# Performance work log

Measured on AMD Instinct MI355X. Metric: run time of the kernel, lower is better.

The kernel has to match this reference:

```python
import jax, jax.numpy as jnp
import numpy as np

P = 1024          # number of projection angles
N = 64            # harmonic order -> 2N+1 = 129 basis functions
K = 7             # temporal basis order -> K+1 = 8 functions
NUM_INSTANCES = 8
L_OUT = 256       # native temporal-function length
M = 512           # g_t.shape[-2]
NB = 2 * N + 1


def _interp_linear(f, out_len):
    # torch F.interpolate(mode='linear', align_corners=False) on a 1D signal f: [L]
    L = f.shape[-1]
    x = (jnp.arange(out_len, dtype=f.dtype) + 0.5) * (L / out_len) - 0.5
    x = jnp.clip(x, 0.0, L - 1)
    x0 = jnp.floor(x).astype(jnp.int32)
    x1 = jnp.minimum(x0 + 1, L - 1)
    w = x - x0.astype(f.dtype)
    return f[x0] * (1.0 - w) + f[x1] * w


def setup_inputs() -> dict:
    key = jax.random.key(0)
    k1, k2, k3 = jax.random.split(key, 3)
    g_t = jax.random.normal(k1, (1, 1, M, 2 * P), dtype=jnp.float32)
    temporal_fcts = jax.random.normal(k2, (1, K + 1, L_OUT), dtype=jnp.float32)
    theta = jax.random.uniform(k3, (P,), dtype=jnp.float32) * jnp.pi
    return {"g_t": g_t, "temporal_fcts": temporal_fcts, "theta": theta}


def reference(g_t, temporal_fcts, theta):
    g_c = g_t.astype(jnp.complex64)                       # [1,1,M,2P]
    n_idx = jnp.arange(NB, dtype=jnp.float32) - N         # (n - N)
    # Theta_mtx[p,n] = exp(1j*(n-N)*theta[p]); symm uses (theta - pi)
    Theta = jnp.exp(1j * n_idx[None, :] * theta[:, None])             # [P, NB] complex64
    Theta_s = jnp.exp(1j * n_idx[None, :] * (theta[:, None] - jnp.pi))  # [P, NB]
    # psi_mtx[k,p]: interpolate each temporal function from L_OUT -> P samples
    psi = jax.vmap(lambda f: _interp_linear(f, P))(temporal_fcts[0])  # [K+1, P] real
    psi_c = psi.astype(jnp.complex64)
    # L1[p, n*(K+1)+k] = Theta[p,n] * psi[k,p]  (top block); symm block below
    top = (Theta[:, :, None] * psi_c.T[:, None, :]).reshape(P, NB * (K + 1))
    bot = (Theta_s[:, :, None] * psi_c.T[:, None, :]).reshape(P, NB * (K + 1))
    L1 = jnp.concatenate([top, bot], axis=0)              # [2P, NB*(K+1)]
    eta = jnp.linalg.pinv(L1) @ jnp.swapaxes(g_c, 2, 3)   # [1,1,NB*(K+1),M]
    g_est = L1 @ eta                                      # [1,1,2P,M]
    # b[m,n,p] = sum_k eta[0,0,n*(K+1)+k,m] * psi[k,p]
    eta_r = eta[0, 0].reshape(NB, K + 1, M)
    b = jnp.einsum('nkm,kp->mnp', eta_r, psi_c)           # [M, NB, P]
    # f_pol_est_s[m,p,i] = sum_n b[m,n, i*P//I] * Theta[p,n]
    sel = (jnp.arange(NUM_INSTANCES) * P) // NUM_INSTANCES
    f_pol_est_s = jnp.einsum('mni,pn->mpi', b[:, :, sel], Theta)  # [M, P, I]
    psi_mtx = psi_c[None]                                  # [1, K+1, P]
    return eta, L1, jnp.swapaxes(g_est, 2, 3), b, f_pol_est_s, psi_mtx
```

## Files before the change

kernel.cpp:

```cpp
#include <hip/hip_runtime.h>

#define NQ 1032
#define NE 520
#define NO 512

#define C_ETA 0
#define C_L1  1056768
#define C_G   5283840
#define C_B   7380992
#define C_F   142647296
#define C_PSI 151035904
#define C_TOTAL 151052288

#define R_ETA 0
#define R_L1  528384
#define R_G   2641920
#define R_B   3690496
#define R_F   71323648
#define R_PSI 75517952

#define SL_PSI32 0
#define SL_THC32 9216
#define SL_THS32 142336
#define SL_BSEL  275456
#define SL_TOTALF 1332224

#define SB_PSI64 0
#define SB_THC64 69632
#define SB_THS64 1130496
#define SB_CT    2191360
#define SB_A0    2262016
#define SB_B0    6592512
#define SB_B1    10856448
#define SB_INVD  15054848
#define SB_LT    15059008
#define SB_RZ    19851328
#define SB_TOTAL 24643648

__device__ inline void tri_it(int e, int& i, int& t){
  i = 0; int base = 0;
  while (base + i + 1 <= e){ base += i + 1; ++i; }
  t = e - base;
}

__global__ __launch_bounds__(256) void k_prep(const float* tf, const float* theta,
    float* psi32, double* psi64, double* thc64, double* ths64,
    float* thc32, float* ths32, float* o_psi, int cpx){
  int idx = blockIdx.x*256 + threadIdx.x;
  if (idx < 8192){
    int k = idx >> 10, p = idx & 1023;
    double x = 0.25*(double)p - 0.375;
    x = fmin(fmax(x, 0.0), 255.0);
    int x0 = (int)x;
    int x1 = min(x0+1, 255);
    double w = x - (double)x0;
    double v = (double)tf[k*256+x0]*(1.0-w) + (double)tf[k*256+x1]*w;
    psi64[k*1024+p] = v;
    float vf = (float)v;
    psi32[k*1024+p] = vf;
    if (cpx){ o_psi[idx*2+0] = vf; o_psi[idx*2+1] = 0.f; }
    else    { o_psi[idx] = vf; }
  } else {
    int j = idx - 8192;
    if (j < 129*1024){
      int n = j >> 10, p = j & 1023;
      double a = (double)(n-64)*(double)theta[p];
      double c = cos(a), s = sin(a);
      thc64[j] = c; ths64[j] = s;
      thc32[j] = (float)c; ths32[j] = (float)s;
    }
  }
}

__global__ __launch_bounds__(256) void k_l1out(const float* tf, const float* theta,
    float* out_l1, int cpx){
  int row = blockIdx.x; int p = row & 1023; int bot = row >> 10;
  __shared__ float cc[129], ss[129], pp[8];
  int tid = threadIdx.x;
  float th = theta[p];
  if (tid < 129){
    float a = (float)(tid - 64) * th;
    cc[tid] = cosf(a); ss[tid] = sinf(a);
  }
  if (tid >= 192 && tid < 200){
    int k = tid - 192;
    float x = 0.25f*(float)p - 0.375f;
    x = fminf(fmaxf(x, 0.f), 255.f);
    int x0 = (int)x;
    int x1 = min(x0+1, 255);
    float w = x - (float)x0;
    pp[k] = tf[k*256+x0]*(1.f-w) + tf[k*256+x1]*w;
  }
  __syncthreads();
  for (int q = tid; q < NQ; q += 256){
    int n = q >> 3, k = q & 7;
    float sg = (bot && (n & 1)) ? -1.f : 1.f;
    float w = pp[k]*sg;
    if (cpx) ((float2*)out_l1)[(size_t)row*NQ + q] = make_float2(cc[n]*w, ss[n]*w);
    else     out_l1[(size_t)row*NQ + q] = cc[n]*w;
  }
}

__global__ __launch_bounds__(256) void k_ctab(const float* theta, const double* psi64, double2* C){
  int t = blockIdx.x; double dd = 2.0*(double)t;
  __shared__ double cs[1024], sn[1024];
  __shared__ double red[4][2];
  int tid = threadIdx.x;
  for (int p = tid; p < 1024; p += 256){ double a = dd*(double)theta[p]; cs[p] = cos(a); sn[p] = sin(a); }
  __syncthreads();
  int lane = tid & 63, wid = tid >> 6;
  for (int k = 0; k < 8; ++k) for (int k2 = k; k2 < 8; ++k2){
    double sr = 0, si = 0;
    for (int p = tid; p < 1024; p += 256){
      double w = psi64[k*1024+p]*psi64[k2*1024+p];
      sr += cs[p]*w; si += sn[p]*w;
    }
    for (int o = 32; o > 0; o >>= 1){ sr += __shfl_down(sr, o, 64); si += __shfl_down(si, o, 64); }
    if (lane == 0){ red[wid][0] = sr; red[wid][1] = si; }
    __syncthreads();
    if (tid == 0){
      double R = red[0][0]+red[1][0]+red[2][0]+red[3][0];
      double I = red[0][1]+red[1][1]+red[2][1]+red[3][1];
      C[t*64 + k*8 + k2] = make_double2(R, I);
      C[t*64 + k2*8 + k] = make_double2(R, I);
    }
    __syncthreads();
  }
}

__global__ __launch_bounds__(256) void k_afill(const double2* C, double2* A){
  int idx = blockIdx.x*256 + threadIdx.x;
  if (idx >= NE*NE) return;
  int r = idx / NE, cix = idx - r*NE;
  int k = r & 7, i = r >> 3, j = cix >> 3, k2 = cix & 7;
  int dt = j - i;
  double2 v;
  if (dt >= 0){ v = C[dt*64 + k*8 + k2]; v.x *= 2.0; v.y *= 2.0; }
  else { v = C[(-dt)*64 + k*8 + k2]; v.x *= 2.0; v.y *= -2.0; }
  A[idx] = v;
}

__global__ __launch_bounds__(256) void k_bgemm(const float* g, const double* thc64, const double* ths64,
    const double* psi64, double2* B0, double2* B1){
  int n = blockIdx.x; int m0 = blockIdx.y * 128;
  int par = n & 1;
  __shared__ float u[64][129];
  __shared__ double cs[64], sn[64], ps[8][64];
  int tid = threadIdx.x;
  int k = tid >> 5, mg = tid & 31;
  double ar[4] = {0,0,0,0}, ai[4] = {0,0,0,0};
  for (int p0 = 0; p0 < 1024; p0 += 64){
    __syncthreads();
    if (tid < 64){ cs[tid] = thc64[n*1024 + p0 + tid]; sn[tid] = ths64[n*1024 + p0 + tid]; }
    for (int e = tid; e < 512; e += 256){ int kk = e >> 6, pp = e & 63; ps[kk][pp] = psi64[kk*1024 + p0 + pp]; }
    for (int e = tid; e < 2048; e += 256){
      int m = e >> 4, p4 = (e & 15) * 4;
      const float4 a = *(const float4*)(g + (size_t)(m0+m)*2048 + p0 + p4);
      const float4 b = *(const float4*)(g + (size_t)(m0+m)*2048 + 1024 + p0 + p4);
      float4 uu;
      if (par){ uu.x = a.x-b.x; uu.y = a.y-b.y; uu.z = a.z-b.z; uu.w = a.w-b.w; }
      else    { uu.x = a.x+b.x; uu.y = a.y+b.y; uu.z = a.z+b.z; uu.w = a.w+b.w; }
      u[p4+0][m] = uu.x; u[p4+1][m] = uu.y; u[p4+2][m] = uu.z; u[p4+3][m] = uu.w;
    }
    __syncthreads();
    for (int p = 0; p < 64; ++p){
      double w = ps[k][p];
      double wr = cs[p]*w, wi = sn[p]*w;
      #pragma unroll
      for (int j = 0; j < 4; ++j){
        double uu = (double)u[p][mg + 32*j];
        ar[j] += wr*uu; ai[j] -= wi*uu;
      }
    }
  }
  int hr = (n >> 1)*8 + k;
  double2* B = par ? B1 : B0;
  #pragma unroll
  for (int j = 0; j < 4; ++j) B[(size_t)hr*512 + m0 + mg + 32*j] = make_double2(ar[j], ai[j]);
}

__global__ __launch_bounds__(256) void k_potrf(double2* A, double* invd, int j0){
  __shared__ double2 T[2145];
  int tid = threadIdx.x;
  for (int e = tid; e < 2145; e += 256){
    int i, t; tri_it(e, i, t);
    T[e] = A[(size_t)(j0+i)*NE + j0 + t];
  }
  __syncthreads();
  for (int j = 0; j < 65; ++j){
    double inv = 1.0 / T[(j*(j+1))/2 + j].x;
    int i = j + 1 + (tid & 63);
    if (i < 65){
      double2 lij = T[(i*(i+1))/2 + j];
      for (int t = j+1+(tid>>6); t <= i; t += 4){
        double2 ltj = T[(t*(t+1))/2 + j];
        double2 a = T[(i*(i+1))/2 + t];
        a.x -= (lij.x*ltj.x + lij.y*ltj.y)*inv;
        a.y -= (lij.y*ltj.x - lij.x*ltj.y)*inv;
        T[(i*(i+1))/2 + t] = a;
      }
    }
    __syncthreads();
  }
  for (int e = tid; e < 2145; e += 256){
    int i, t; tri_it(e, i, t);
    double dinv = 1.0 / sqrt(T[(t*(t+1))/2 + t].x);
    double2 v = T[e]; v.x *= dinv; v.y *= dinv;
    A[(size_t)(j0+i)*NE + j0 + t] = v;
    if (i == t) invd[j0+i] = dinv;
  }
}

__global__ __launch_bounds__(256) void k_trsm(double2* A, const double* invd, int j0){
  int lane = threadIdx.x & 63, wid = threadIdx.x >> 6;
  int rg = j0 + 65 + blockIdx.x*4 + wid;
  if (rg >= NE) return;
  double2 a0 = A[(size_t)rg*NE + j0 + lane];
  double2 a64 = (lane == 0) ? A[(size_t)rg*NE + j0 + 64] : make_double2(0,0);
  for (int c = 0; c < 65; ++c){
    double xr, xi;
    if (c < 64){ xr = __shfl(a0.x, c, 64); xi = __shfl(a0.y, c, 64); }
    else { xr = __shfl(a64.x, 0, 64); xi = __shfl(a64.y, 0, 64); }
    double iv = invd[j0 + c];
    xr *= iv; xi *= iv;
    if (c < 64){ if (lane == c){ a0.x = xr; a0.y = xi; } }
    else if (lane == 0){ a64.x = xr; a64.y = xi; }
    if (lane > c){
      double2 l = A[(size_t)(j0+lane)*NE + j0 + c];
      a0.x -= xr*l.x + xi*l.y; a0.y -= xi*l.x - xr*l.y;
    }
    if (lane == 0 && c < 64){
      double2 l = A[(size_t)(j0+64)*NE + j0 + c];
      a64.x -= xr*l.x + xi*l.y; a64.y -= xi*l.x - xr*l.y;
    }
  }
  A[(size_t)rg*NE + j0 + lane] = a0;
  if (lane == 0) A[(size_t)rg*NE + j0 + 64] = a64;
}

__global__ __launch_bounds__(256) void k_syrk(double2* A, int j0){
  if (blockIdx.y > blockIdx.x) return;
  int j1 = j0 + 65;
  int i0 = j1 + blockIdx.x*32, t0 = j1 + blockIdx.y*32;
  __shared__ double2 Li[32][17];
  __shared__ double2 Lt[32][17];
  int tid = threadIdx.x;
  int oi = tid >> 3, tj = (tid & 7)*4;
  double2 acc[4] = {make_double2(0,0),make_double2(0,0),make_double2(0,0),make_double2(0,0)};
  for (int c0 = 0; c0 < 65; c0 += 16){
    int cw = min(16, 65 - c0);
    __syncthreads();
    for (int e = tid; e < 512; e += 256){
      int r = e >> 4, c = e & 15;
      double2 zi = make_double2(0,0), zt = zi;
      if (c < cw){
        if (i0 + r < NE) zi = A[(size_t)(i0+r)*NE + j0 + c0 + c];
        if (t0 + r < NE) zt = A[(size_t)(t0+r)*NE + j0 + c0 + c];
      }
      Li[r][c] = zi; Lt[r][c] = zt;
    }
    __syncthreads();
    for (int c = 0; c < cw; ++c){
      double2 li = Li[oi][c];
      #pragma unroll
      for (int j = 0; j < 4; ++j){
        double2 lt = Lt[tj+j][c];
        acc[j].x += li.x*lt.x + li.y*lt.y;
        acc[j].y += li.y*lt.x - li.x*lt.y;
      }
    }
  }
  int gi = i0 + oi;
  if (gi < NE){
    #pragma unroll
    for (int j = 0; j < 4; ++j){
      int gt = t0 + tj + j;
      if (gt < NE && gt <= gi){
        double2 v = A[(size_t)gi*NE + gt];
        v.x -= acc[j].x; v.y -= acc[j].y;
        A[(size_t)gi*NE + gt] = v;
      }
    }
  }
}

__global__ __launch_bounds__(256) void k_tr(const double2* A, double2* LT){
  __shared__ double2 tl[32][33];
  int bc = blockIdx.x*32;
  int bt = blockIdx.y*32;
  int lx = threadIdx.x & 31, ly = threadIdx.x >> 5;
  #pragma unroll
  for (int rr = 0; rr < 32; rr += 8){
    int t = bt + ly + rr, c = bc + lx;
    double2 v = make_double2(0,0);
    if (t < NE && c < NE && t > c) v = A[(size_t)t*NE + c];
    tl[ly+rr][lx] = v;
  }
  __syncthreads();
  #pragma unroll
  for (int rr = 0; rr < 32; rr += 8){
    int c = bc + ly + rr, t = bt + lx;
    if (c < NE) LT[(size_t)c*576 + t] = tl[lx][ly+rr];
  }
}

__global__ __launch_bounds__(256) void k_rz(const double2* A, double2* RZ){
  int idx = blockIdx.x*256 + threadIdx.x;
  if (idx >= NE*576) return;
  int c = idx / 576, t = idx - c*576;
  double2 v = (t < c) ? A[(size_t)c*NE + t] : make_double2(0,0);
  RZ[idx] = v;
}

__global__ __launch_bounds__(256) void k_solve(const double2* LT, const double2* RZ,
                                               const double* invd,
                                               double2* B0, double2* B1){
  int tid = threadIdx.x; int lane = tid & 63; int wid = tid >> 6;
  int w = blockIdx.x*4 + wid;
  int sys = (w >= 256) ? 1 : 0;
  int c0 = (sys ? (w - 256) : w) * 2;
  int n = sys ? NO : NE;
  double2* B = sys ? B1 : B0;
  double2 y[9][2];
  #pragma unroll
  for (int r = 0; r < 9; ++r){
    int t = r*64 + lane;
    #pragma unroll
    for (int j = 0; j < 2; ++j)
      y[r][j] = (t < n) ? B[(size_t)t*512 + c0 + j] : make_double2(0,0);
  }

  double2 Lc[9], Ln[9];

  #pragma unroll
  for (int r = 0; r < 9; ++r) Lc[r] = LT[(size_t)0*576 + r*64 + lane];
  #pragma unroll
  for (int rr = 0; rr < 9; ++rr){
    if (rr*64 < n){
      int cend = min(n, rr*64 + 64);
      for (int c = rr*64; c < cend; ++c){
        if (c + 1 < n){
          #pragma unroll
          for (int r = 0; r < 9; ++r) Ln[r] = LT[(size_t)(c+1)*576 + r*64 + lane];
        }
        int la = c & 63;
        double iv = invd[c];
        double xr[2], xi[2];
        #pragma unroll
        for (int j = 0; j < 2; ++j){
          xr[j] = __shfl(y[rr][j].x, la, 64)*iv;
          xi[j] = __shfl(y[rr][j].y, la, 64)*iv;
        }
        if (lane == la){
          #pragma unroll
          for (int j = 0; j < 2; ++j){ y[rr][j].x = xr[j]; y[rr][j].y = xi[j]; }
        }
        #pragma unroll
        for (int r = 0; r < 9; ++r){
          if (r >= rr){
            double2 l = Lc[r];
            #pragma unroll
            for (int j = 0; j < 2; ++j){
              y[r][j].x -= l.x*xr[j] - l.y*xi[j];
              y[r][j].y -= l.x*xi[j] + l.y*xr[j];
            }
          }
        }
        #pragma unroll
        for (int r = 0; r < 9; ++r) Lc[r] = Ln[r];
      }
    }
  }

  #pragma unroll
  for (int r = 0; r < 9; ++r) Lc[r] = RZ[(size_t)(n-1)*576 + r*64 + lane];
  #pragma unroll
  for (int rr = 8; rr >= 0; --rr){
    if (rr*64 < n){
      int cstart = min(n, rr*64 + 64) - 1;
      for (int c = cstart; c >= rr*64; --c){
        if (c > 0){
          #pragma unroll
          for (int r = 0; r < 9; ++r) Ln[r] = RZ[(size_t)(c-1)*576 + r*64 + lane];
        }
        int la = c & 63;
        double iv = invd[c];
        double xr[2], xi[2];
        #pragma unroll
        for (int j = 0; j < 2; ++j){
          xr[j] = __shfl(y[rr][j].x, la, 64)*iv;
          xi[j] = __shfl(y[rr][j].y, la, 64)*iv;
        }
        if (lane == la){
          #pragma unroll
          for (int j = 0; j < 2; ++j){ y[rr][j].x = xr[j]; y[rr][j].y = xi[j]; }
        }
        #pragma unroll
        for (int r = 0; r < 9; ++r){
          if (r <= rr){
            double2 l = Lc[r];
            #pragma unroll
            for (int j = 0; j < 2; ++j){
              y[r][j].x -= l.x*xr[j] + l.y*xi[j];
              y[r][j].y -= l.x*xi[j] - l.y*xr[j];
            }
          }
        }
        #pragma unroll
        for (int r = 0; r < 9; ++r) Lc[r] = Ln[r];
      }
    }
  }

  #pragma unroll
  for (int r = 0; r < 9; ++r){
    int t = r*64 + lane;
    if (t < n){
      #pragma unroll
      for (int j = 0; j < 2; ++j) B[(size_t)t*512 + c0 + j] = y[r][j];
    }
  }
}

__global__ __launch_bounds__(256) void k_eta(const double2* B0, const double2* B1,
                                             float* out_eta, int cpx){
  int idx = blockIdx.x*256 + threadIdx.x;
  if (idx >= NQ*512) return;
  int q = idx >> 9;
  int m = idx & 511;
  int n = q >> 3, k = q & 7;
  const double2* B = (n & 1) ? B1 : B0;
  int hr = (n >> 1)*8 + k;
  double2 v = B[(size_t)hr*512 + m];
  if (cpx) ((float2*)out_eta)[idx] = make_float2((float)v.x, (float)v.y);
  else     out_eta[idx] = (float)v.x;
}

__global__ __launch_bounds__(256) void k_gestb(const double2* B0, const double2* B1,
    const float* psi32, const float* thc32, const float* ths32,
    float* out_b, float* out_g, float2* BSEL, int cpx){
  int m = blockIdx.x; int p = blockIdx.y*256 + threadIdx.x;
  __shared__ float4 eL4[516];
  float2* eL2 = (float2*)eL4;
  for (int e = threadIdx.x; e < NQ; e += 256){
    int n = e >> 3, k = e & 7;
    const double2* B = (n & 1) ? B1 : B0;
    double2 v = B[(size_t)((n >> 1)*8 + k)*512 + m];
    eL2[e] = make_float2((float)v.x, (float)v.y);
  }
  __syncthreads();
  float pr[8];
  #pragma unroll
  for (int k = 0; k < 8; ++k) pr[k] = psi32[k*1024+p];
  float aEx=0, aEy=0, aOx=0, aOy=0;
  size_t bbase = (size_t)m*129*1024 + p;
  for (int n = 0; n < 129; ++n){
    float c = thc32[n*1024+p], s = ths32[n*1024+p];
    float4 e0 = eL4[n*4+0], e1 = eL4[n*4+1], e2 = eL4[n*4+2], e3 = eL4[n*4+3];
    float br = e0.x*pr[0] + e0.z*pr[1] + e1.x*pr[2] + e1.z*pr[3]
             + e2.x*pr[4] + e2.z*pr[5] + e3.x*pr[6] + e3.z*pr[7];
    float bi = e0.y*pr[0] + e0.w*pr[1] + e1.y*pr[2] + e1.w*pr[3]
             + e2.y*pr[4] + e2.w*pr[5] + e3.y*pr[6] + e3.w*pr[7];
    if (cpx) ((float2*)out_b)[bbase + (size_t)n*1024] = make_float2(br, bi);
    else     out_b[bbase + (size_t)n*1024] = br;
    if ((p & 127) == 0) BSEL[(size_t)m*NQ + n*8 + (p >> 7)] = make_float2(br, bi);
    float tr = c*br - s*bi, ti = c*bi + s*br;
    if (n & 1){ aOx += tr; aOy += ti; } else { aEx += tr; aEy += ti; }
  }
  if (cpx){
    ((float2*)out_g)[(size_t)m*2048 + p]        = make_float2(aEx+aOx, aEy+aOy);
    ((float2*)out_g)[(size_t)m*2048 + p + 1024] = make_float2(aEx-aOx, aEy-aOy);
  } else {
    out_g[(size_t)m*2048 + p]        = aEx+aOx;
    out_g[(size_t)m*2048 + p + 1024] = aEx-aOx;
  }
}

__global__ __launch_bounds__(256) void k_fpol(const float2* BSEL, const float* thc32,
    const float* ths32, float* out_f, int cpx){
  int m = blockIdx.x; int p = blockIdx.y*256 + threadIdx.x;
  __shared__ float4 bs4[516];
  float2* bs2 = (float2*)bs4;
  for (int e = threadIdx.x; e < NQ; e += 256) bs2[e] = BSEL[(size_t)m*NQ + e];
  __syncthreads();
  float ar[8] = {0,0,0,0,0,0,0,0}, ai[8] = {0,0,0,0,0,0,0,0};
  for (int n = 0; n < 129; ++n){
    float c = thc32[n*1024+p], s = ths32[n*1024+p];
    #pragma unroll
    for (int jj = 0; jj < 4; ++jj){
      float4 v = bs4[n*4+jj];
      ar[2*jj]   += c*v.x - s*v.y;  ai[2*jj]   += c*v.y + s*v.x;
      ar[2*jj+1] += c*v.z - s*v.w;  ai[2*jj+1] += c*v.w + s*v.z;
    }
  }
  if (cpx){
    float4* o = (float4*)(out_f + ((size_t)m*1024 + p)*16);
    o[0] = make_float4(ar[0],ai[0],ar[1],ai[1]);
    o[1] = make_float4(ar[2],ai[2],ar[3],ai[3]);
    o[2] = make_float4(ar[4],ai[4],ar[5],ai[5]);
    o[3] = make_float4(ar[6],ai[6],ar[7],ai[7]);
  } else {
    float4* o = (float4*)(out_f + ((size_t)m*1024 + p)*8);
    o[0] = make_float4(ar[0],ar[1],ar[2],ar[3]);
    o[1] = make_float4(ar[4],ar[5],ar[6],ar[7]);
  }
}

extern "C" void kernel_launch(void* const* d_in, const int* in_sizes, int n_in,
                              void* d_out, int out_size, void* d_ws, size_t ws_size,
                              hipStream_t stream){
  const float* g     = (const float*)d_in[0];
  const float* tf    = (const float*)d_in[1];
  const float* theta = (const float*)d_in[2];
  float* out = (float*)d_out;

  int cpx = (out_size >= C_TOTAL) ? 1 : 0;
  float* o_eta = out + (cpx ? C_ETA : R_ETA);
  float* o_l1  = out + (cpx ? C_L1  : R_L1);
  float* o_g   = out + (cpx ? C_G   : R_G);
  float* o_b   = out + (cpx ? C_B   : R_B);
  float* o_f   = out + (cpx ? C_F   : R_F);
  float* o_psi = out + (cpx ? C_PSI : R_PSI);

  size_t need = (size_t)SB_TOTAL + (size_t)SL_TOTALF*4 + 4096;
  char*  sb;
  float* sl;
  if (ws_size >= need){
    sb = (char*)d_ws;
    sl = (float*)((char*)d_ws + SB_TOTAL);
  } else {
    sb = (char*)o_b;
    sl = o_l1;
  }
  float*   psi32 = sl + SL_PSI32;
  float*   thc32 = sl + SL_THC32;
  float*   ths32 = sl + SL_THS32;
  float2*  BSEL  = (float2*)(sl + SL_BSEL);
  double*  psi64 = (double*)(sb + SB_PSI64);
  double*  thc64 = (double*)(sb + SB_THC64);
  double*  ths64 = (double*)(sb + SB_THS64);
  double2* Ct    = (double2*)(sb + SB_CT);
  double2* A0    = (double2*)(sb + SB_A0);
  double2* B0    = (double2*)(sb + SB_B0);
  double2* B1    = (double2*)(sb + SB_B1);
  double*  INVD  = (double*)(sb + SB_INVD);
  double2* LT    = (double2*)(sb + SB_LT);
  double2* RZ    = (double2*)(sb + SB_RZ);

  k_prep <<<548, 256, 0, stream>>>(tf, theta, psi32, psi64, thc64, ths64, thc32, ths32, o_psi, cpx);
  k_ctab <<<65, 256, 0, stream>>>(theta, psi64, Ct);
  k_afill<<<1057, 256, 0, stream>>>(Ct, A0);
  k_bgemm<<<dim3(129,4), 256, 0, stream>>>(g, thc64, ths64, psi64, B0, B1);
  for (int s = 0; s < 8; ++s){
    k_potrf<<<1, 256, 0, stream>>>(A0, INVD, s*65);
    int rem = NE - 65*(s+1);
    if (rem > 0){
      k_trsm<<<(rem+3)/4, 256, 0, stream>>>(A0, INVD, s*65);
      int nt = (rem+31)/32;
      k_syrk<<<dim3(nt,nt), 256, 0, stream>>>(A0, s*65);
    }
  }
  k_tr   <<<dim3(17,18), 256, 0, stream>>>(A0, LT);
  k_rz   <<<(NE*576 + 255)/256, 256, 0, stream>>>(A0, RZ);
  k_solve<<<128, 256, 0, stream>>>(LT, RZ, INVD, B0, B1);
  k_eta  <<<2064, 256, 0, stream>>>(B0, B1, o_eta, cpx);
  k_gestb<<<dim3(512,4), 256, 0, stream>>>(B0, B1, psi32, thc32, ths32, o_b, o_g, BSEL, cpx);
  k_fpol <<<dim3(512,4), 256, 0, stream>>>(BSEL, thc32, ths32, o_f, cpx);
  k_l1out<<<2048, 256, 0, stream>>>(tf, theta, o_l1, cpx);
}
```

Baseline: 1.957 ms.

## Stage triangular-solve factor columns in shared memory and halve per-wave RHS

The forward/backward triangular solve now has one right-hand side per wave instead of two, and the grid is doubled. The four waves of a block share double-buffered shared-memory tiles of four factor columns each, so every column is read from global memory once per block rather than once per wave. Rows above the current diagonal block are skipped when loading. The TRSM kernel also stages the 65x65 diagonal panel and the inverse diagonals in shared memory, and tri_it uses a sqrt-based index guess. The cost is block-wide barriers every four columns and one block per CU from the launch bounds.

```diff
diff --git a/kernel.cpp b/kernel.cpp
--- a/kernel.cpp
+++ b/kernel.cpp
@@ -38,9 +38,11 @@
 #define SB_TOTAL 24643648
 
 __device__ inline void tri_it(int e, int& i, int& t){
-  i = 0; int base = 0;
-  while (base + i + 1 <= e){ base += i + 1; ++i; }
-  t = e - base;
+  int ii = (int)((sqrt(8.0*(double)e + 1.0) - 1.0) * 0.5);
+  int base = (ii*(ii+1)) >> 1;
+  while (base + ii + 1 <= e){ base += ii + 1; ++ii; }
+  while (base > e){ base -= ii; --ii; }
+  i = ii; t = e - base;
 }
 
 __global__ __launch_bounds__(256) void k_prep(const float* tf, const float* theta,
@@ -212,7 +214,16 @@
 }
 
 __global__ __launch_bounds__(256) void k_trsm(double2* A, const double* invd, int j0){
-  int lane = threadIdx.x & 63, wid = threadIdx.x >> 6;
+  __shared__ double2 Lp[65*65];
+  __shared__ double ivp[65];
+  int tid = threadIdx.x;
+  for (int e = tid; e < 65*65; e += 256){
+    int i = e / 65, c = e - i*65;
+    Lp[c*65 + i] = A[(size_t)(j0+i)*NE + j0 + c];
+  }
+  if (tid < 65) ivp[tid] = invd[j0 + tid];
+  __syncthreads();
+  int lane = tid & 63, wid = tid >> 6;
   int rg = j0 + 65 + blockIdx.x*4 + wid;
   if (rg >= NE) return;
   double2 a0 = A[(size_t)rg*NE + j0 + lane];
@@ -221,16 +232,16 @@
     double xr, xi;
     if (c < 64){ xr = __shfl(a0.x, c, 64); xi = __shfl(a0.y, c, 64); }
     else { xr = __shfl(a64.x, 0, 64); xi = __shfl(a64.y, 0, 64); }
-    double iv = invd[j0 + c];
+    double iv = ivp[c];
     xr *= iv; xi *= iv;
     if (c < 64){ if (lane == c){ a0.x = xr; a0.y = xi; } }
     else if (lane == 0){ a64.x = xr; a64.y = xi; }
     if (lane > c){
-      double2 l = A[(size_t)(j0+lane)*NE + j0 + c];
+      double2 l = Lp[c*65 + lane];
       a0.x -= xr*l.x + xi*l.y; a0.y -= xi*l.x - xr*l.y;
     }
     if (lane == 0 && c < 64){
-      double2 l = A[(size_t)(j0+64)*NE + j0 + c];
+      double2 l = Lp[c*65 + 64];
       a64.x -= xr*l.x + xi*l.y; a64.y -= xi*l.x - xr*l.y;
     }
   }
@@ -312,113 +323,153 @@
   RZ[idx] = v;
 }
 
-__global__ __launch_bounds__(256) void k_solve(const double2* LT, const double2* RZ,
-                                               const double* invd,
-                                               double2* B0, double2* B1){
-  int tid = threadIdx.x; int lane = tid & 63; int wid = tid >> 6;
-  int w = blockIdx.x*4 + wid;
-  int sys = (w >= 256) ? 1 : 0;
-  int c0 = (sys ? (w - 256) : w) * 2;
+template<int RR>
+__device__ __forceinline__ void fwd4(double2* y, const double2* Lsc, const double* ivc, int cb, int lane){
+  constexpr int NR64 = (9 - RR)*64;
+  #pragma unroll
+  for (int cc = 0; cc < 4; ++cc){
+    int la = (cb + cc) & 63;
+    double iv = ivc[cc];
+    double xr = __shfl(y[RR].x, la, 64)*iv;
+    double xi = __shfl(y[RR].y, la, 64)*iv;
+    if (lane == la){ y[RR].x = xr; y[RR].y = xi; }
+    #pragma unroll
+    for (int r = RR; r < 9; ++r){
+      double2 l = Lsc[cc*NR64 + (r-RR)*64 + lane];
+      y[r].x -= l.x*xr - l.y*xi;
+      y[r].y -= l.x*xi + l.y*xr;
+    }
+  }
+}
+
+template<int RR>
+__device__ __forceinline__ void bwd4(double2* y, const double2* Lsc, const double* ivc, int cb, int lane){
+  constexpr int NR64 = (RR + 1)*64;
+  #pragma unroll
+  for (int cc = 3; cc >= 0; --cc){
+    int la = (cb + cc) & 63;
+    double iv = ivc[cc];
+    double xr = __shfl(y[RR].x, la, 64)*iv;
+    double xi = __shfl(y[RR].y, la, 64)*iv;
+    if (lane == la){ y[RR].x = xr; y[RR].y = xi; }
+    #pragma unroll
+    for (int r = 0; r <= RR; ++r){
+      double2 l = Lsc[cc*NR64 + r*64 + lane];
+      y[r].x -= l.x*xr + l.y*xi;
+      y[r].y -= l.x*xi - l.y*xr;
+    }
+  }
+}
+
+__global__ __launch_bounds__(256,1) void k_solve(const double2* __restrict__ LT, const double2* __restrict__ RZ,
+                                                 const double* __restrict__ invd,
+                                                 double2* B0, double2* B1){
+  __shared__ double2 Ls[2][4*576];
+  __shared__ double ivb[2][4];
+  int tid = threadIdx.x, lane = tid & 63, z = tid >> 6;
+  int w = blockIdx.x*4 + z;
+  int sys = (w >= 512) ? 1 : 0;
+  int c0 = sys ? (w - 512) : w;
   int n = sys ? NO : NE;
   double2* B = sys ? B1 : B0;
-  double2 y[9][2];
+  double2 y[9];
   #pragma unroll
   for (int r = 0; r < 9; ++r){
     int t = r*64 + lane;
-    #pragma unroll
-    for (int j = 0; j < 2; ++j)
-      y[r][j] = (t < n) ? B[(size_t)t*512 + c0 + j] : make_double2(0,0);
-  }
-
-  double2 Lc[9], Ln[9];
-
-  #pragma unroll
-  for (int r = 0; r < 9; ++r) Lc[r] = LT[(size_t)0*576 + r*64 + lane];
-  #pragma unroll
-  for (int rr = 0; rr < 9; ++rr){
-    if (rr*64 < n){
-      int cend = min(n, rr*64 + 64);
-      for (int c = rr*64; c < cend; ++c){
-        if (c + 1 < n){
-          #pragma unroll
-          for (int r = 0; r < 9; ++r) Ln[r] = LT[(size_t)(c+1)*576 + r*64 + lane];
-        }
-        int la = c & 63;
-        double iv = invd[c];
-        double xr[2], xi[2];
-        #pragma unroll
-        for (int j = 0; j < 2; ++j){
-          xr[j] = __shfl(y[rr][j].x, la, 64)*iv;
-          xi[j] = __shfl(y[rr][j].y, la, 64)*iv;
-        }
-        if (lane == la){
-          #pragma unroll
-          for (int j = 0; j < 2; ++j){ y[rr][j].x = xr[j]; y[rr][j].y = xi[j]; }
-        }
-        #pragma unroll
-        for (int r = 0; r < 9; ++r){
-          if (r >= rr){
-            double2 l = Lc[r];
-            #pragma unroll
-            for (int j = 0; j < 2; ++j){
-              y[r][j].x -= l.x*xr[j] - l.y*xi[j];
-              y[r][j].y -= l.x*xi[j] + l.y*xr[j];
-            }
-          }
-        }
-        #pragma unroll
-        for (int r = 0; r < 9; ++r) Lc[r] = Ln[r];
-      }
-    }
-  }
-
-  #pragma unroll
-  for (int r = 0; r < 9; ++r) Lc[r] = RZ[(size_t)(n-1)*576 + r*64 + lane];
-  #pragma unroll
-  for (int rr = 8; rr >= 0; --rr){
-    if (rr*64 < n){
-      int cstart = min(n, rr*64 + 64) - 1;
-      for (int c = cstart; c >= rr*64; --c){
-        if (c > 0){
-          #pragma unroll
-          for (int r = 0; r < 9; ++r) Ln[r] = RZ[(size_t)(c-1)*576 + r*64 + lane];
-        }
-        int la = c & 63;
-        double iv = invd[c];
-        double xr[2], xi[2];
-        #pragma unroll
-        for (int j = 0; j < 2; ++j){
-          xr[j] = __shfl(y[rr][j].x, la, 64)*iv;
-          xi[j] = __shfl(y[rr][j].y, la, 64)*iv;
-        }
-        if (lane == la){
-          #pragma unroll
-          for (int j = 0; j < 2; ++j){ y[rr][j].x = xr[j]; y[rr][j].y = xi[j]; }
-        }
-        #pragma unroll
-        for (int r = 0; r < 9; ++r){
-          if (r <= rr){
-            double2 l = Lc[r];
-            #pragma unroll
-            for (int j = 0; j < 2; ++j){
-              y[r][j].x -= l.x*xr[j] + l.y*xi[j];
-              y[r][j].y -= l.x*xi[j] - l.y*xr[j];
-            }
-          }
-        }
-        #pragma unroll
-        for (int r = 0; r < 9; ++r) Lc[r] = Ln[r];
-      }
+    y[r] = (t < n) ? B[(size_t)t*512 + c0] : make_double2(0,0);
+  }
+  int nch = n >> 2;
+  double2 stg[9]; double ivs = 0;
+
+  {
+    size_t ga = (size_t)z*576 + lane;
+    #pragma unroll
+    for (int i = 0; i < 9; ++i) stg[i] = LT[ga + i*64];
+    if (tid < 4) ivs = invd[tid];
+    #pragma unroll
+    for (int i = 0; i < 9; ++i) Ls[0][z*576 + i*64 + lane] = stg[i];
+    if (tid < 4) ivb[0][tid] = ivs;
+  }
+  for (int k = 0; k < nch; ++k){
+    int cur = k & 1;
+    __syncthreads();
+    int rrn = (k+1) >> 4;
+    if (k+1 < nch){
+      int nr = 9 - rrn;
+      size_t ga = (size_t)((k+1)*4 + z)*576 + rrn*64 + lane;
+      #pragma unroll
+      for (int i = 0; i < 9; ++i) if (i < nr) stg[i] = LT[ga + i*64];
+      if (tid < 4) ivs = invd[(k+1)*4 + tid];
+    }
+    int cb = k*4;
+    const double2* Lsc = &Ls[cur][0];
+    const double* ivc = &ivb[cur][0];
+    switch (k >> 4){
+      case 0: fwd4<0>(y, Lsc, ivc, cb, lane); break;
+      case 1: fwd4<1>(y, Lsc, ivc, cb, lane); break;
+      case 2: fwd4<2>(y, Lsc, ivc, cb, lane); break;
+      case 3: fwd4<3>(y, Lsc, ivc, cb, lane); break;
+      case 4: fwd4<4>(y, Lsc, ivc, cb, lane); break;
+      case 5: fwd4<5>(y, Lsc, ivc, cb, lane); break;
+      case 6: fwd4<6>(y, Lsc, ivc, cb, lane); break;
+      case 7: fwd4<7>(y, Lsc, ivc, cb, lane); break;
+      default: fwd4<8>(y, Lsc, ivc, cb, lane); break;
+    }
+    if (k+1 < nch){
+      int nr = 9 - rrn, nr64 = (9 - rrn)*64;
+      #pragma unroll
+      for (int i = 0; i < 9; ++i) if (i < nr) Ls[cur^1][z*nr64 + i*64 + lane] = stg[i];
+      if (tid < 4) ivb[cur^1][tid] = ivs;
+    }
+  }
+
+  {
+    int kb = nch - 1;
+    int nr = (kb >> 4) + 1, nr64 = nr*64;
+    size_t ga = (size_t)(kb*4 + z)*576 + lane;
+    #pragma unroll
+    for (int i = 0; i < 9; ++i) if (i < nr) stg[i] = RZ[ga + i*64];
+    if (tid < 4) ivs = invd[kb*4 + tid];
+    #pragma unroll
+    for (int i = 0; i < 9; ++i) if (i < nr) Ls[0][z*nr64 + i*64 + lane] = stg[i];
+    if (tid < 4) ivb[0][tid] = ivs;
+  }
+  for (int k = nch-1; k >= 0; --k){
+    int cur = (nch-1 - k) & 1;
+    __syncthreads();
+    if (k > 0){
+      int nr = ((k-1) >> 4) + 1;
+      size_t ga = (size_t)((k-1)*4 + z)*576 + lane;
+      #pragma unroll
+      for (int i = 0; i < 9; ++i) if (i < nr) stg[i] = RZ[ga + i*64];
+      if (tid < 4) ivs = invd[(k-1)*4 + tid];
+    }
+    int cb = k*4;
+    const double2* Lsc = &Ls[cur][0];
+    const double* ivc = &ivb[cur][0];
+    switch (k >> 4){
+      case 0: bwd4<0>(y, Lsc, ivc, cb, lane); break;
+      case 1: bwd4<1>(y, Lsc, ivc, cb, lane); break;
+      case 2: bwd4<2>(y, Lsc, ivc, cb, lane); break;
+      case 3: bwd4<3>(y, Lsc, ivc, cb, lane); break;
+      case 4: bwd4<4>(y, Lsc, ivc, cb, lane); break;
+      case 5: bwd4<5>(y, Lsc, ivc, cb, lane); break;
+      case 6: bwd4<6>(y, Lsc, ivc, cb, lane); break;
+      case 7: bwd4<7>(y, Lsc, ivc, cb, lane); break;
+      default: bwd4<8>(y, Lsc, ivc, cb, lane); break;
+    }
+    if (k > 0){
+      int nr = ((k-1) >> 4) + 1, nr64 = nr*64;
+      #pragma unroll
+      for (int i = 0; i < 9; ++i) if (i < nr) Ls[cur^1][z*nr64 + i*64 + lane] = stg[i];
+      if (tid < 4) ivb[cur^1][tid] = ivs;
     }
   }
 
   #pragma unroll
   for (int r = 0; r < 9; ++r){
     int t = r*64 + lane;
-    if (t < n){
-      #pragma unroll
-      for (int j = 0; j < 2; ++j) B[(size_t)t*512 + c0 + j] = y[r][j];
-    }
+    if (t < n) B[(size_t)t*512 + c0] = y[r];
   }
 }
 
@@ -562,7 +613,7 @@
   }
   k_tr   <<<dim3(17,18), 256, 0, stream>>>(A0, LT);
   k_rz   <<<(NE*576 + 255)/256, 256, 0, stream>>>(A0, RZ);
-  k_solve<<<128, 256, 0, stream>>>(LT, RZ, INVD, B0, B1);
+  k_solve<<<256, 256, 0, stream>>>(LT, RZ, INVD, B0, B1);
   k_eta  <<<2064, 256, 0, stream>>>(B0, B1, o_eta, cpx);
   k_gestb<<<dim3(512,4), 256, 0, stream>>>(B0, B1, psi32, thc32, ths32, o_b, o_g, BSEL, cpx);
   k_fpol <<<dim3(512,4), 256, 0, stream>>>(BSEL, thc32, ths32, o_f, cpx);
```

After: 2.250 ms. +15.0%, slower.
